# Optimization experiments

Hardware: AMD Instinct MI355X
Metric: run time of the kernel (lower is better)

The kernel has to match this reference:

```python
import jax, jax.numpy as jnp
import numpy as np

N_EMBD = 1024
N_HEAD = 16
HEAD_SIZE = N_EMBD // N_HEAD
EPS = 1e-5


def layernorm(x, g, b):
    mu = jnp.mean(x, axis=-1, keepdims=True)
    var = jnp.var(x, axis=-1, keepdims=True)
    return (x - mu) * jax.lax.rsqrt(var + EPS) * g + b


def setup_inputs() -> dict:
    key = jax.random.key(0)
    ks = jax.random.split(key, 12)
    s = 0.02
    C = N_EMBD
    return {
        "x": jax.random.normal(ks[0], (2, 2048, C), dtype=jnp.float32),
        "Wq": jax.random.normal(ks[1], (C, C), dtype=jnp.float32) * s,
        "Wk": jax.random.normal(ks[2], (C, C), dtype=jnp.float32) * s,
        "Wv": jax.random.normal(ks[3], (C, C), dtype=jnp.float32) * s,
        "Wo": jax.random.normal(ks[4], (C, C), dtype=jnp.float32) * s,
        "bo": jnp.zeros((C,), dtype=jnp.float32),
        "W1": jax.random.normal(ks[5], (C, 4 * C), dtype=jnp.float32) * s,
        "b1": jnp.zeros((4 * C,), dtype=jnp.float32),
        "W2": jax.random.normal(ks[6], (4 * C, C), dtype=jnp.float32) * s,
        "b2": jnp.zeros((C,), dtype=jnp.float32),
        "ln1_g": jnp.ones((C,), dtype=jnp.float32),
        "ln1_b": jnp.zeros((C,), dtype=jnp.float32),
        "ln2_g": jnp.ones((C,), dtype=jnp.float32),
        "ln2_b": jnp.zeros((C,), dtype=jnp.float32),
    }


def reference(x, Wq, Wk, Wv, Wo, bo, W1, b1, W2, b2, ln1_g, ln1_b, ln2_g, ln2_b):
    B, T, C = x.shape
    H, Dh = N_HEAD, HEAD_SIZE

    # --- self-attention branch ---
    h = layernorm(x, ln1_g, ln1_b)
    q = (h @ Wq).reshape(B, T, H, Dh)
    k = (h @ Wk).reshape(B, T, H, Dh)
    v = (h @ Wv).reshape(B, T, H, Dh)

    # NOTE: original scales by C**-0.5 (n_embd), not head_size**-0.5
    scale = C ** (-0.5)
    scores = jnp.einsum("bqhd,bkhd->bhqk", q, k) * scale  # [B,H,T,T]
    causal = jnp.tril(jnp.ones((T, T), dtype=bool))
    scores = jnp.where(causal, scores, -jnp.inf)
    wei = jax.nn.softmax(scores, axis=-1)
    attn = jnp.einsum("bhqk,bkhd->bqhd", wei, v).reshape(B, T, C)
    x = x + attn @ Wo + bo

    # --- MLP branch ---
    h2 = layernorm(x, ln2_g, ln2_b)
    ff = jax.nn.relu(h2 @ W1 + b1) @ W2 + b2
    return x + ff
```

## Files before the change

### kernel.cpp

```cpp
#include <hip/hip_runtime.h>

typedef unsigned short u16;
typedef __bf16 bf16;
typedef bf16 bf16x8 __attribute__((ext_vector_type(8)));
typedef float f32x4 __attribute__((ext_vector_type(4)));


__device__ __forceinline__ u16 f2bf(float f) {
  bf16 b = (bf16)f;
  return __builtin_bit_cast(u16, b);
}

__device__ __forceinline__ float fexp2(float x) {
#if __has_builtin(__builtin_amdgcn_exp2f)
  return __builtin_amdgcn_exp2f(x);
#else
  return exp2f(x);
#endif
}

__device__ __forceinline__ void gll16(void* lds, const void* g) {
  __builtin_amdgcn_global_load_lds((__attribute__((address_space(1))) void*)g,
                                   (__attribute__((address_space(3))) void*)lds,
                                   16, 0, 0);
}

__device__ __forceinline__ f32x4 mfma16(bf16x8 a, bf16x8 b, f32x4 c) {
  return __builtin_amdgcn_mfma_f32_16x16x32_bf16(a, b, c, 0, 0, 0);
}


__global__ __launch_bounds__(256)
void transpose_all(const float* __restrict__ Wq, const float* __restrict__ Wk,
                   const float* __restrict__ Wv, const float* __restrict__ Wo,
                   const float* __restrict__ W1, const float* __restrict__ W2,
                   u16* __restrict__ WqT, u16* __restrict__ WkT,
                   u16* __restrict__ WvT, u16* __restrict__ WoT,
                   u16* __restrict__ W1T, u16* __restrict__ W2T) {
  __shared__ float tile[32][33];
  const int id = blockIdx.x;
  const float* src;
  u16* dst;
  int R, C, t;
  if (id < 4096) {
    const int w = id >> 10;
    t = id & 1023; R = 1024; C = 1024;
    src = w == 0 ? Wq : w == 1 ? Wk : w == 2 ? Wv : Wo;
    dst = w == 0 ? WqT : w == 1 ? WkT : w == 2 ? WvT : WoT;
  } else if (id < 8192) {
    t = id - 4096; R = 1024; C = 4096; src = W1; dst = W1T;
  } else {
    t = id - 8192; R = 4096; C = 1024; src = W2; dst = W2T;
  }
  const int tilesx = C >> 5;
  const int c0 = (t % tilesx) * 32, r0 = (t / tilesx) * 32;
  const int tx = threadIdx.x, ty = threadIdx.y;
#pragma unroll
  for (int i = 0; i < 4; ++i)
    tile[ty + i * 8][tx] = src[(size_t)(r0 + ty + i * 8) * C + c0 + tx];
  __syncthreads();
#pragma unroll
  for (int i = 0; i < 4; ++i)
    dst[(size_t)(c0 + ty + i * 8) * R + r0 + tx] = f2bf(tile[tx][ty + i * 8]);
}


__global__ __launch_bounds__(256)
void ln_kernel(const float* __restrict__ x, const float* __restrict__ g,
               const float* __restrict__ bb, u16* __restrict__ h) {
  const int row = blockIdx.x;
  const int tid = threadIdx.x;
  const float4 xv = ((const float4*)(x + (size_t)row * 1024))[tid];
  float s = xv.x + xv.y + xv.z + xv.w;
  float q = xv.x * xv.x + xv.y * xv.y + xv.z * xv.z + xv.w * xv.w;
#pragma unroll
  for (int m = 1; m < 64; m <<= 1) {
    s += __shfl_xor(s, m);
    q += __shfl_xor(q, m);
  }
  __shared__ float ss[4], qq[4];
  const int wid = tid >> 6, lane = tid & 63;
  if (lane == 0) { ss[wid] = s; qq[wid] = q; }
  __syncthreads();
  s = ss[0] + ss[1] + ss[2] + ss[3];
  q = qq[0] + qq[1] + qq[2] + qq[3];
  const float mean = s * (1.0f / 1024.0f);
  const float var = q * (1.0f / 1024.0f) - mean * mean;
  const float rs = rsqrtf(var + 1e-5f);
  const float4 gv = ((const float4*)g)[tid];
  const float4 bv = ((const float4*)bb)[tid];
  ushort4 o;
  o.x = f2bf((xv.x - mean) * rs * gv.x + bv.x);
  o.y = f2bf((xv.y - mean) * rs * gv.y + bv.y);
  o.z = f2bf((xv.z - mean) * rs * gv.z + bv.z);
  o.w = f2bf((xv.w - mean) * rs * gv.w + bv.w);
  ((ushort4*)(h + (size_t)row * 1024))[tid] = o;
}


__device__ __forceinline__ void xcd_swizzle(int& bx, int& by, int& bz) {
  const int gx = gridDim.x, gy = gridDim.y;
  const int nwg = gx * gy * (int)gridDim.z;
  int flat = (int)blockIdx.x + gx * ((int)blockIdx.y + gy * (int)blockIdx.z);
  flat = (flat & 7) * (nwg >> 3) + (flat >> 3);
  bx = flat % gx;
  const int rem = flat / gx;
  by = rem % gy;
  bz = rem / gy;
}


template <int EPI>
__global__ __launch_bounds__(256)
void gemm_bt(const u16* __restrict__ A, const u16* __restrict__ Bt,
             const float* __restrict__ bias,
             void* __restrict__ O0, void* __restrict__ O1, void* __restrict__ O2,
             int M, int N, int K) {
  __shared__ __align__(16) u16 Alds[3][128 * 32];
  __shared__ __align__(16) u16 Blds[3][128 * 32];
  const int tid = threadIdx.x;
  const int lane = tid & 63, wid = tid >> 6;
  const int rl = lane & 15, kg = lane >> 4;
  const int ksw = (rl >> 1) & 3;
  int bx, by, bz;
  xcd_swizzle(bx, by, bz);
  const int m0 = by * 128, n0 = bx * 128;
  f32x4 acc[4][4];
#pragma unroll
  for (int i = 0; i < 4; ++i)
#pragma unroll
    for (int j = 0; j < 4; ++j) acc[i][j] = (f32x4){0.f, 0.f, 0.f, 0.f};
  const int wr = wid >> 1, wc = wid & 1;
  const int c0 = wid * 2, c1 = wid * 2 + 1;
  const int srow0 = c0 * 16 + (lane >> 2);
  const int srow1 = c1 * 16 + (lane >> 2);
  const int skol = (((lane & 3) ^ ((lane >> 3) & 3))) * 8;

#define STAGE_BT(buf, k0)                                                      \
  {                                                                            \
    gll16(Alds[buf] + c0 * 512, A + (size_t)(m0 + srow0) * K + (k0) + skol);   \
    gll16(Alds[buf] + c1 * 512, A + (size_t)(m0 + srow1) * K + (k0) + skol);   \
    gll16(Blds[buf] + c0 * 512, Bt + (size_t)(n0 + srow0) * K + (k0) + skol);  \
    gll16(Blds[buf] + c1 * 512, Bt + (size_t)(n0 + srow1) * K + (k0) + skol);  \
  }

  const int nt = K >> 5;
  STAGE_BT(0, 0);
  STAGE_BT(1, 32);
  int cur = 0;
  for (int t = 0; t < nt; ++t) {
    if (t + 1 < nt)
      asm volatile("s_waitcnt vmcnt(4)" ::: "memory");
    else
      asm volatile("s_waitcnt vmcnt(0)" ::: "memory");
    __builtin_amdgcn_s_barrier();
    if (t + 2 < nt) {
      const int nxt = cur >= 1 ? cur - 1 : cur + 2;
      STAGE_BT(nxt, (t + 2) << 5);
    }
    bf16x8 af[4], bfr[4];
#pragma unroll
    for (int m = 0; m < 4; ++m)
      af[m] = *(const bf16x8*)(Alds[cur] + (wr * 64 + m * 16 + rl) * 32 +
                               (kg ^ ksw) * 8);
#pragma unroll
    for (int n = 0; n < 4; ++n)
      bfr[n] = *(const bf16x8*)(Blds[cur] + (wc * 64 + n * 16 + rl) * 32 +
                                (kg ^ ksw) * 8);
    __builtin_amdgcn_s_setprio(1);
#pragma unroll
    for (int m = 0; m < 4; ++m)
#pragma unroll
      for (int n = 0; n < 4; ++n)
        acc[m][n] = mfma16(af[m], bfr[n], acc[m][n]);
    __builtin_amdgcn_s_setprio(0);
    cur = cur + 1 == 3 ? 0 : cur + 1;
  }
#undef STAGE_BT

#pragma unroll
  for (int m = 0; m < 4; ++m) {
#pragma unroll
    for (int n = 0; n < 4; ++n) {
      const int col = n0 + wc * 64 + n * 16 + rl;
      const int row0 = m0 + wr * 64 + m * 16 + kg * 4;
      if (EPI == 0) {
        const int seg = col >> 10;
        const int lc = col & 1023;
        if (seg == 2) {
          u16* vt = (u16*)O2;
          const size_t off =
              ((size_t)((row0 >> 11) * 16 + (lc >> 6)) * 64 + (lc & 63)) * 2048 +
              (row0 & 2047);
          ushort4 pk = {f2bf(acc[m][n][0]), f2bf(acc[m][n][1]),
                        f2bf(acc[m][n][2]), f2bf(acc[m][n][3])};
          *(ushort4*)(vt + off) = pk;
        } else {
          u16* o = (u16*)(seg == 0 ? O0 : O1);
#pragma unroll
          for (int r = 0; r < 4; ++r)
            o[(size_t)(row0 + r) * 1024 + lc] = f2bf(acc[m][n][r]);
        }
      } else {
        const float bv = bias[col];
#pragma unroll
        for (int r = 0; r < 4; ++r) {
          float v = acc[m][n][r] + bv;
          v = v > 0.f ? v : 0.f;
          ((u16*)O0)[(size_t)(row0 + r) * N + col] = f2bf(v);
        }
      }
    }
  }
}


__global__ __launch_bounds__(256)
void gemm64(const u16* __restrict__ A, const u16* __restrict__ Bt,
            const float* __restrict__ bias, const float* __restrict__ res,
            float* __restrict__ O, int M, int N, int K) {
  __shared__ __align__(16) u16 Alds[3][64 * 64];
  __shared__ __align__(16) u16 Blds[3][128 * 64];
  const int tid = threadIdx.x;
  const int lane = tid & 63, wid = tid >> 6;
  const int rl = lane & 15, kg = lane >> 4;
  int bx, by, bz;
  xcd_swizzle(bx, by, bz);
  const int m0 = by * 64, n0 = bx * 128;
  f32x4 acc[2][4];
#pragma unroll
  for (int i = 0; i < 2; ++i)
#pragma unroll
    for (int j = 0; j < 4; ++j) acc[i][j] = (f32x4){0.f, 0.f, 0.f, 0.f};
  const int wr = wid >> 1, wc = wid & 1;
  const int lrow = lane >> 3;
  const int lslot = lane & 7;

#define SRCA(base_r, k0)                                                       \
  (A + (size_t)(m0 + (base_r) + lrow) * K + (k0) +                             \
   ((lslot ^ (((base_r) + lrow) & 7)) * 8))
#define SRCB(base_r, k0)                                                       \
  (Bt + (size_t)(n0 + (base_r) + lrow) * K + (k0) +                            \
   ((lslot ^ (((base_r) + lrow) & 7)) * 8))

#define STAGE_64(buf, k0)                                                      \
  {                                                                            \
    gll16(Alds[buf] + (wid * 16 + 0) * 64, SRCA(wid * 16 + 0, k0));            \
    gll16(Alds[buf] + (wid * 16 + 8) * 64, SRCA(wid * 16 + 8, k0));            \
    gll16(Blds[buf] + (wid * 32 + 0) * 64, SRCB(wid * 32 + 0, k0));            \
    gll16(Blds[buf] + (wid * 32 + 8) * 64, SRCB(wid * 32 + 8, k0));            \
    gll16(Blds[buf] + (wid * 32 + 16) * 64, SRCB(wid * 32 + 16, k0));          \
    gll16(Blds[buf] + (wid * 32 + 24) * 64, SRCB(wid * 32 + 24, k0));          \
  }

  const int nt = K >> 6;
  STAGE_64(0, 0);
  STAGE_64(1, 64);
  int cur = 0;
  for (int t = 0; t < nt; ++t) {
    if (t + 1 < nt)
      asm volatile("s_waitcnt vmcnt(6)" ::: "memory");
    else
      asm volatile("s_waitcnt vmcnt(0)" ::: "memory");
    __builtin_amdgcn_s_barrier();
    if (t + 2 < nt) {
      const int nxt = cur >= 1 ? cur - 1 : cur + 2;
      STAGE_64(nxt, (t + 2) << 6);
    }
    bf16x8 af[2][2], bfr[4][2];
#pragma unroll
    for (int m = 0; m < 2; ++m) {
      const int row = wr * 32 + m * 16 + rl;
#pragma unroll
      for (int kf = 0; kf < 2; ++kf)
        af[m][kf] = *(const bf16x8*)(Alds[cur] + row * 64 +
                                     ((kf * 4 + kg) ^ (row & 7)) * 8);
    }
#pragma unroll
    for (int n = 0; n < 4; ++n) {
      const int row = wc * 64 + n * 16 + rl;
#pragma unroll
      for (int kf = 0; kf < 2; ++kf)
        bfr[n][kf] = *(const bf16x8*)(Blds[cur] + row * 64 +
                                      ((kf * 4 + kg) ^ (row & 7)) * 8);
    }
    __builtin_amdgcn_s_setprio(1);
#pragma unroll
    for (int m = 0; m < 2; ++m)
#pragma unroll
      for (int n = 0; n < 4; ++n) {
        acc[m][n] = mfma16(af[m][0], bfr[n][0], acc[m][n]);
        acc[m][n] = mfma16(af[m][1], bfr[n][1], acc[m][n]);
      }
    __builtin_amdgcn_s_setprio(0);
    cur = cur + 1 == 3 ? 0 : cur + 1;
  }
#undef STAGE_64
#undef SRCA
#undef SRCB

#pragma unroll
  for (int m = 0; m < 2; ++m) {
#pragma unroll
    for (int n = 0; n < 4; ++n) {
      const int col = n0 + wc * 64 + n * 16 + rl;
      const int row0 = m0 + wr * 32 + m * 16 + kg * 4;
      const float bv = bias[col];
#pragma unroll
      for (int r = 0; r < 4; ++r) {
        const int row = row0 + r;
        O[(size_t)row * N + col] =
            acc[m][n][r] + bv + res[(size_t)row * N + col];
      }
    }
  }
}


#define SC2 0.045084220027780106f

__device__ __forceinline__ void attn_range(
    const u16* __restrict__ qg, const u16* __restrict__ kgl,
    const u16* __restrict__ vtb, size_t rowb, int cb, char* plw,
    int rl, int kg, int q0, int kvb, int kve, bool mask_last,
    f32x4 (&ot)[2][4], float (&lrun)[2]) {
  if (kvb >= kve) return;
  const int swz = (rl & 7) << 4;
  bf16x8 qf[2][2];
#pragma unroll
  for (int m = 0; m < 2; ++m) {
    const u16* qp = qg + (rowb + q0 + m * 16 + rl) * 1024 + cb + kg * 8;
    qf[m][0] = *(const bf16x8*)(qp);
    qf[m][1] = *(const bf16x8*)(qp + 32);
  }

  bf16x8 ka[4][2], kb[4][2];
#define LOADK(dst, kvi)                                                        \
  {                                                                            \
    const u16* krow = kgl + (rowb + (kvi) * 64 + rl) * 1024 + cb + kg * 8;     \
    _Pragma("unroll") for (int n = 0; n < 4; ++n) {                            \
      dst[n][0] = *(const bf16x8*)(krow + (size_t)n * 16 * 1024);              \
      dst[n][1] = *(const bf16x8*)(krow + (size_t)n * 16 * 1024 + 32);         \
    }                                                                          \
  }

#define BODY(kf, kvi)                                                          \
  {                                                                            \
    const int kv0 = (kvi) * 64;                                                \
    const u16* vrow = vtb + (size_t)rl * 2048 + kv0 + kg * 8;                  \
    bf16x8 vfr[4][2];                                                          \
    _Pragma("unroll") for (int dt = 0; dt < 4; ++dt) {                         \
      vfr[dt][0] = *(const bf16x8*)(vrow + (size_t)dt * 16 * 2048);            \
      vfr[dt][1] = *(const bf16x8*)(vrow + (size_t)dt * 16 * 2048 + 32);       \
    }                                                                          \
    const bool domask = mask_last && ((kvi) == kve - 1);                       \
    _Pragma("unroll") for (int m = 0; m < 2; ++m) {                            \
      f32x4 s[4];                                                              \
      __builtin_amdgcn_s_setprio(1);                                           \
      _Pragma("unroll") for (int n = 0; n < 4; ++n) {                          \
        f32x4 t = (f32x4){0.f, 0.f, 0.f, 0.f};                                 \
        t = mfma16(kf[n][0], qf[m][0], t);                                     \
        t = mfma16(kf[n][1], qf[m][1], t);                                     \
        s[n] = t;                                                              \
      }                                                                        \
      __builtin_amdgcn_s_setprio(0);                                           \
      if (domask) {                                                            \
        const int qrow = q0 + m * 16 + rl;                                     \
        _Pragma("unroll") for (int n = 0; n < 4; ++n)                          \
            _Pragma("unroll") for (int r = 0; r < 4; ++r) {                    \
          const int tk = kv0 + n * 16 + 4 * kg + r;                            \
          s[n][r] = (tk > qrow) ? -3e38f : s[n][r];                            \
        }                                                                      \
      }                                                                        \
      float ps = 0.f;                                                          \
      _Pragma("unroll") for (int n = 0; n < 4; ++n) {                          \
        const float p0 = fexp2(__builtin_fmaf(s[n][0], SC2, -8.f));            \
        const float p1 = fexp2(__builtin_fmaf(s[n][1], SC2, -8.f));            \
        const float p2 = fexp2(__builtin_fmaf(s[n][2], SC2, -8.f));            \
        const float p3 = fexp2(__builtin_fmaf(s[n][3], SC2, -8.f));            \
        ps += (p0 + p1) + (p2 + p3);                                           \
        ushort4 pk = {f2bf(p0), f2bf(p1), f2bf(p2), f2bf(p3)};                 \
        *(ushort4*)(plw + m * 2048 + ((rl * 128 + n * 32 + kg * 8) ^ swz)) =   \
            pk;                                                                \
      }                                                                        \
      lrun[m] += ps;                                                           \
    }                                                                          \
    _Pragma("unroll") for (int m = 0; m < 2; ++m) {                            \
      const bf16x8 pf0 =                                                       \
          *(const bf16x8*)(plw + m * 2048 + ((rl * 128 + kg * 16) ^ swz));     \
      const bf16x8 pf1 = *(const bf16x8*)(plw + m * 2048 +                     \
                                          ((rl * 128 + 64 + kg * 16) ^ swz));  \
      __builtin_amdgcn_s_setprio(1);                                           \
      _Pragma("unroll") for (int dt = 0; dt < 4; ++dt) {                       \
        ot[m][dt] = mfma16(vfr[dt][0], pf0, ot[m][dt]);                        \
        ot[m][dt] = mfma16(vfr[dt][1], pf1, ot[m][dt]);                        \
      }                                                                        \
      __builtin_amdgcn_s_setprio(0);                                           \
    }                                                                          \
  }

  LOADK(ka, kvb);
  int kv = kvb;
  for (;;) {
    if (kv + 1 < kve) LOADK(kb, kv + 1);
    BODY(ka, kv);
    ++kv;
    if (kv >= kve) break;
    if (kv + 1 < kve) LOADK(ka, kv + 1);
    BODY(kb, kv);
    ++kv;
    if (kv >= kve) break;
  }
#undef LOADK
#undef BODY
}

__global__ __launch_bounds__(128)
void attn_kernel(const u16* __restrict__ qg, const u16* __restrict__ kgl,
                 const u16* __restrict__ vtg, u16* __restrict__ og) {
  const int tid = threadIdx.x, lane = tid & 63, wid = tid >> 6;
  const int rl = lane & 15, kg = lane >> 4;
  const int flat = blockIdx.x;
  const int bh = (flat & 7) * 4 + ((flat >> 3) & 3);
  const int pr = flat >> 5;
  const int jA = pr, jB = 63 - pr;
  const int nA = (jA >> 1) + 1, nB = (jB >> 1) + 1;
  const int a = (nB - nA) >> 1;
  const size_t rowb = (size_t)(bh >> 4) * 2048;
  const int cb = (bh & 15) * 64;
  const u16* vtb = vtg + (size_t)bh * 64 * 2048;

  __shared__ __align__(16) char Pl[2][4096];
  __shared__ __align__(16) float MrgO[2][4][64][4];
  __shared__ float MrgL[2][16];
  char* plw = Pl[wid];

  f32x4 ot[2][4];
  float lrun[2] = {0.f, 0.f};
#pragma unroll
  for (int m = 0; m < 2; ++m)
#pragma unroll
    for (int dt = 0; dt < 4; ++dt) ot[m][dt] = (f32x4){0.f, 0.f, 0.f, 0.f};

  if (wid == 0) {
    attn_range(qg, kgl, vtb, rowb, cb, plw, rl, kg, jA * 32, 0, nA, true,
               ot, lrun);
#pragma unroll
    for (int m = 0; m < 2; ++m) {
      lrun[m] += __shfl_xor(lrun[m], 16);
      lrun[m] += __shfl_xor(lrun[m], 32);
      const float inv = 1.f / lrun[m];
      u16* orow = og + (rowb + jA * 32 + m * 16 + rl) * 1024 + cb;
#pragma unroll
      for (int dt = 0; dt < 4; ++dt) {
        ushort4 ok = {f2bf(ot[m][dt][0] * inv), f2bf(ot[m][dt][1] * inv),
                      f2bf(ot[m][dt][2] * inv), f2bf(ot[m][dt][3] * inv)};
        *(ushort4*)(orow + dt * 16 + 4 * kg) = ok;
      }
      lrun[m] = 0.f;
#pragma unroll
      for (int dt = 0; dt < 4; ++dt) ot[m][dt] = (f32x4){0.f, 0.f, 0.f, 0.f};
    }
    attn_range(qg, kgl, vtb, rowb, cb, plw, rl, kg, jB * 32, 0, a, false,
               ot, lrun);
  } else {
    attn_range(qg, kgl, vtb, rowb, cb, plw, rl, kg, jB * 32, a, nB, true,
               ot, lrun);
#pragma unroll
    for (int m = 0; m < 2; ++m) {
      lrun[m] += __shfl_xor(lrun[m], 16);
      lrun[m] += __shfl_xor(lrun[m], 32);
#pragma unroll
      for (int dt = 0; dt < 4; ++dt)
        *(f32x4*)(&MrgO[m][dt][lane][0]) = ot[m][dt];
      if (kg == 0) MrgL[m][rl] = lrun[m];
    }
  }
  __syncthreads();
  if (wid == 0) {
#pragma unroll
    for (int m = 0; m < 2; ++m) {
      lrun[m] += __shfl_xor(lrun[m], 16);
      lrun[m] += __shfl_xor(lrun[m], 32);
      const float inv = 1.f / (lrun[m] + MrgL[m][rl]);
      u16* orow = og + (rowb + jB * 32 + m * 16 + rl) * 1024 + cb;
#pragma unroll
      for (int dt = 0; dt < 4; ++dt) {
        const f32x4 o1 = *(const f32x4*)(&MrgO[m][dt][lane][0]);
        ushort4 ok;
#pragma unroll
        for (int r = 0; r < 4; ++r)
          ((u16*)&ok)[r] = f2bf((ot[m][dt][r] + o1[r]) * inv);
        *(ushort4*)(orow + dt * 16 + 4 * kg) = ok;
      }
    }
  }
}


extern "C" void kernel_launch(void* const* d_in, const int* in_sizes, int n_in,
                              void* d_out, int out_size, void* d_ws, size_t ws_size,
                              hipStream_t stream) {
  const float* x    = (const float*)d_in[0];
  const float* Wq   = (const float*)d_in[1];
  const float* Wk   = (const float*)d_in[2];
  const float* Wv   = (const float*)d_in[3];
  const float* Wo   = (const float*)d_in[4];
  const float* bo   = (const float*)d_in[5];
  const float* W1   = (const float*)d_in[6];
  const float* b1   = (const float*)d_in[7];
  const float* W2   = (const float*)d_in[8];
  const float* b2   = (const float*)d_in[9];
  const float* ln1g = (const float*)d_in[10];
  const float* ln1b = (const float*)d_in[11];
  const float* ln2g = (const float*)d_in[12];
  const float* ln2b = (const float*)d_in[13];
  float* out = (float*)d_out;

  char* ws = (char*)d_ws;
  const size_t MB = 1024 * 1024;
  u16* WqT  = (u16*)(ws + 0 * MB);
  u16* WoT  = (u16*)(ws + 6 * MB);
  u16* W1T  = (u16*)(ws + 8 * MB);
  u16* W2T  = (u16*)(ws + 16 * MB);
  u16* h    = (u16*)(ws + 24 * MB);
  u16* q    = (u16*)(ws + 32 * MB);
  u16* k    = (u16*)(ws + 40 * MB);
  u16* vt   = (u16*)(ws + 48 * MB);
  u16* attn = (u16*)(ws + 56 * MB);
  float* x1 = (float*)(ws + 64 * MB);
  u16* ff1  = (u16*)(ws + 32 * MB);
  u16* WkT  = WqT + 1024 * 1024;
  u16* WvT  = WqT + 2 * 1024 * 1024;

  dim3 tblk(32, 8);
  transpose_all<<<12288, tblk, 0, stream>>>(Wq, Wk, Wv, Wo, W1, W2,
                                            WqT, WkT, WvT, WoT, W1T, W2T);

  ln_kernel<<<4096, 256, 0, stream>>>(x, ln1g, ln1b, h);

  gemm_bt<0><<<dim3(24, 32), 256, 0, stream>>>(h, WqT, nullptr,
                                               q, k, vt, 4096, 3072, 1024);

  attn_kernel<<<1024, 128, 0, stream>>>(q, k, vt, attn);

  gemm64<<<dim3(8, 64), 256, 0, stream>>>(attn, WoT, bo, x, x1,
                                          4096, 1024, 1024);

  ln_kernel<<<4096, 256, 0, stream>>>(x1, ln2g, ln2b, h);

  gemm_bt<1><<<dim3(32, 32), 256, 0, stream>>>(h, W1T, b1, ff1, ff1, ff1,
                                               4096, 4096, 1024);

  gemm64<<<dim3(8, 64), 256, 0, stream>>>(ff1, W2T, b2, x1, out,
                                          4096, 1024, 4096);
}
```

Baseline: 253.3 us.

## Software-pipeline attention QK^T ahead of softmax and store residual x1 in bf16

The attention inner loop is restructured so the QK^T MFMAs for the next KV tile run while the current tile's softmax and PV are processed. K loads are issued two tiles ahead, with V loaded per step, to overlap memory latency with compute at the cost of extra score registers. Separately, the post-attention residual x1 is stored as bf16 instead of fp32, which halves its write and two reads but adds rounding error to the residual stream.

```diff
diff --git a/kernel.cpp b/kernel.cpp
--- a/kernel.cpp
+++ b/kernel.cpp
@@ -9,6 +9,10 @@
 __device__ __forceinline__ u16 f2bf(float f) {
   bf16 b = (bf16)f;
   return __builtin_bit_cast(u16, b);
+}
+
+__device__ __forceinline__ float b2f(u16 u) {
+  return __uint_as_float(((unsigned)u) << 16);
 }
 
 __device__ __forceinline__ float fexp2(float x) {
@@ -65,12 +69,19 @@
 }
 
 
+template <int BF16IN>
 __global__ __launch_bounds__(256)
-void ln_kernel(const float* __restrict__ x, const float* __restrict__ g,
+void ln_kernel(const void* __restrict__ xin, const float* __restrict__ g,
                const float* __restrict__ bb, u16* __restrict__ h) {
   const int row = blockIdx.x;
   const int tid = threadIdx.x;
-  const float4 xv = ((const float4*)(x + (size_t)row * 1024))[tid];
+  float4 xv;
+  if (BF16IN) {
+    const ushort4 u = ((const ushort4*)((const u16*)xin + (size_t)row * 1024))[tid];
+    xv.x = b2f(u.x); xv.y = b2f(u.y); xv.z = b2f(u.z); xv.w = b2f(u.w);
+  } else {
+    xv = ((const float4*)((const float*)xin + (size_t)row * 1024))[tid];
+  }
   float s = xv.x + xv.y + xv.z + xv.w;
   float q = xv.x * xv.x + xv.y * xv.y + xv.z * xv.z + xv.w * xv.w;
 #pragma unroll
@@ -215,10 +226,11 @@
 }
 
 
+template <int EPI>
 __global__ __launch_bounds__(256)
 void gemm64(const u16* __restrict__ A, const u16* __restrict__ Bt,
-            const float* __restrict__ bias, const float* __restrict__ res,
-            float* __restrict__ O, int M, int N, int K) {
+            const float* __restrict__ bias, const void* __restrict__ res,
+            void* __restrict__ O, int M, int N, int K) {
   __shared__ __align__(16) u16 Alds[3][64 * 64];
   __shared__ __align__(16) u16 Blds[3][128 * 64];
   const int tid = threadIdx.x;
@@ -309,8 +321,13 @@
 #pragma unroll
       for (int r = 0; r < 4; ++r) {
         const int row = row0 + r;
-        O[(size_t)row * N + col] =
-            acc[m][n][r] + bv + res[(size_t)row * N + col];
+        if (EPI == 0) {
+          const float rv = ((const float*)res)[(size_t)row * N + col];
+          ((u16*)O)[(size_t)row * N + col] = f2bf(acc[m][n][r] + bv + rv);
+        } else {
+          const float rv = b2f(((const u16*)res)[(size_t)row * N + col]);
+          ((float*)O)[(size_t)row * N + col] = acc[m][n][r] + bv + rv;
+        }
       }
     }
   }
@@ -334,7 +351,9 @@
     qf[m][1] = *(const bf16x8*)(qp + 32);
   }
 
-  bf16x8 ka[4][2], kb[4][2];
+  bf16x8 ka[4][2], kb[4][2], vf[4][2];
+  f32x4 sa[2][4], sb[2][4];
+
 #define LOADK(dst, kvi)                                                        \
   {                                                                            \
     const u16* krow = kgl + (rowb + (kvi) * 64 + rl) * 1024 + cb + kg * 8;     \
@@ -344,40 +363,47 @@
     }                                                                          \
   }
 
-#define BODY(kf, kvi)                                                          \
+#define LOADV(kvi)                                                             \
+  {                                                                            \
+    const u16* vrow = vtb + (size_t)rl * 2048 + (kvi) * 64 + kg * 8;           \
+    _Pragma("unroll") for (int dt = 0; dt < 4; ++dt) {                         \
+      vf[dt][0] = *(const bf16x8*)(vrow + (size_t)dt * 16 * 2048);             \
+      vf[dt][1] = *(const bf16x8*)(vrow + (size_t)dt * 16 * 2048 + 32);        \
+    }                                                                          \
+  }
+
+#define QKC(S, KF)                                                             \
+  {                                                                            \
+    __builtin_amdgcn_s_setprio(1);                                             \
+    _Pragma("unroll") for (int m = 0; m < 2; ++m)                              \
+        _Pragma("unroll") for (int n = 0; n < 4; ++n) {                        \
+      f32x4 t = (f32x4){0.f, 0.f, 0.f, 0.f};                                   \
+      t = mfma16(KF[n][0], qf[m][0], t);                                       \
+      t = mfma16(KF[n][1], qf[m][1], t);                                       \
+      S[m][n] = t;                                                             \
+    }                                                                          \
+    __builtin_amdgcn_s_setprio(0);                                             \
+  }
+
+#define SMAX(S, kvi)                                                           \
   {                                                                            \
     const int kv0 = (kvi) * 64;                                                \
-    const u16* vrow = vtb + (size_t)rl * 2048 + kv0 + kg * 8;                  \
-    bf16x8 vfr[4][2];                                                          \
-    _Pragma("unroll") for (int dt = 0; dt < 4; ++dt) {                         \
-      vfr[dt][0] = *(const bf16x8*)(vrow + (size_t)dt * 16 * 2048);            \
-      vfr[dt][1] = *(const bf16x8*)(vrow + (size_t)dt * 16 * 2048 + 32);       \
-    }                                                                          \
     const bool domask = mask_last && ((kvi) == kve - 1);                       \
     _Pragma("unroll") for (int m = 0; m < 2; ++m) {                            \
-      f32x4 s[4];                                                              \
-      __builtin_amdgcn_s_setprio(1);                                           \
-      _Pragma("unroll") for (int n = 0; n < 4; ++n) {                          \
-        f32x4 t = (f32x4){0.f, 0.f, 0.f, 0.f};                                 \
-        t = mfma16(kf[n][0], qf[m][0], t);                                     \
-        t = mfma16(kf[n][1], qf[m][1], t);                                     \
-        s[n] = t;                                                              \
-      }                                                                        \
-      __builtin_amdgcn_s_setprio(0);                                           \
       if (domask) {                                                            \
         const int qrow = q0 + m * 16 + rl;                                     \
         _Pragma("unroll") for (int n = 0; n < 4; ++n)                          \
             _Pragma("unroll") for (int r = 0; r < 4; ++r) {                    \
           const int tk = kv0 + n * 16 + 4 * kg + r;                            \
-          s[n][r] = (tk > qrow) ? -3e38f : s[n][r];                            \
+          S[m][n][r] = (tk > qrow) ? -3e38f : S[m][n][r];                      \
         }                                                                      \
       }                                                                        \
       float ps = 0.f;                                                          \
       _Pragma("unroll") for (int n = 0; n < 4; ++n) {                          \
-        const float p0 = fexp2(__builtin_fmaf(s[n][0], SC2, -8.f));            \
-        const float p1 = fexp2(__builtin_fmaf(s[n][1], SC2, -8.f));            \
-        const float p2 = fexp2(__builtin_fmaf(s[n][2], SC2, -8.f));            \
-        const float p3 = fexp2(__builtin_fmaf(s[n][3], SC2, -8.f));            \
+        const float p0 = fexp2(__builtin_fmaf(S[m][n][0], SC2, -8.f));         \
+        const float p1 = fexp2(__builtin_fmaf(S[m][n][1], SC2, -8.f));         \
+        const float p2 = fexp2(__builtin_fmaf(S[m][n][2], SC2, -8.f));         \
+        const float p3 = fexp2(__builtin_fmaf(S[m][n][3], SC2, -8.f));         \
         ps += (p0 + p1) + (p2 + p3);                                           \
         ushort4 pk = {f2bf(p0), f2bf(p1), f2bf(p2), f2bf(p3)};                 \
         *(ushort4*)(plw + m * 2048 + ((rl * 128 + n * 32 + kg * 8) ^ swz)) =   \
@@ -385,6 +411,10 @@
       }                                                                        \
       lrun[m] += ps;                                                           \
     }                                                                          \
+  }
+
+#define PVC()                                                                  \
+  {                                                                            \
     _Pragma("unroll") for (int m = 0; m < 2; ++m) {                            \
       const bf16x8 pf0 =                                                       \
           *(const bf16x8*)(plw + m * 2048 + ((rl * 128 + kg * 16) ^ swz));     \
@@ -392,27 +422,40 @@
                                           ((rl * 128 + 64 + kg * 16) ^ swz));  \
       __builtin_amdgcn_s_setprio(1);                                           \
       _Pragma("unroll") for (int dt = 0; dt < 4; ++dt) {                       \
-        ot[m][dt] = mfma16(vfr[dt][0], pf0, ot[m][dt]);                        \
-        ot[m][dt] = mfma16(vfr[dt][1], pf1, ot[m][dt]);                        \
+        ot[m][dt] = mfma16(vf[dt][0], pf0, ot[m][dt]);                         \
+        ot[m][dt] = mfma16(vf[dt][1], pf1, ot[m][dt]);                         \
       }                                                                        \
       __builtin_amdgcn_s_setprio(0);                                           \
     }                                                                          \
   }
 
+#define STEP(SC_, SN_, KN_, KC_, kvi)                                          \
+  {                                                                            \
+    LOADV(kvi);                                                                \
+    SMAX(SC_, kvi);                                                            \
+    if ((kvi) + 1 < kve) QKC(SN_, KN_);                                        \
+    if ((kvi) + 2 < kve) LOADK(KC_, (kvi) + 2);                                \
+    PVC();                                                                     \
+  }
+
   LOADK(ka, kvb);
+  if (kvb + 1 < kve) LOADK(kb, kvb + 1);
+  QKC(sa, ka);
   int kv = kvb;
   for (;;) {
-    if (kv + 1 < kve) LOADK(kb, kv + 1);
-    BODY(ka, kv);
+    STEP(sa, sb, kb, ka, kv);
     ++kv;
     if (kv >= kve) break;
-    if (kv + 1 < kve) LOADK(ka, kv + 1);
-    BODY(kb, kv);
+    STEP(sb, sa, ka, kb, kv);
     ++kv;
     if (kv >= kve) break;
   }
 #undef LOADK
-#undef BODY
+#undef LOADV
+#undef QKC
+#undef SMAX
+#undef PVC
+#undef STEP
 }
 
 __global__ __launch_bounds__(128)
@@ -528,7 +571,7 @@
   u16* k    = (u16*)(ws + 40 * MB);
   u16* vt   = (u16*)(ws + 48 * MB);
   u16* attn = (u16*)(ws + 56 * MB);
-  float* x1 = (float*)(ws + 64 * MB);
+  u16* x1b  = (u16*)(ws + 64 * MB);
   u16* ff1  = (u16*)(ws + 32 * MB);
   u16* WkT  = WqT + 1024 * 1024;
   u16* WvT  = WqT + 2 * 1024 * 1024;
@@ -537,21 +580,21 @@
   transpose_all<<<12288, tblk, 0, stream>>>(Wq, Wk, Wv, Wo, W1, W2,
                                             WqT, WkT, WvT, WoT, W1T, W2T);
 
-  ln_kernel<<<4096, 256, 0, stream>>>(x, ln1g, ln1b, h);
+  ln_kernel<0><<<4096, 256, 0, stream>>>(x, ln1g, ln1b, h);
 
   gemm_bt<0><<<dim3(24, 32), 256, 0, stream>>>(h, WqT, nullptr,
                                                q, k, vt, 4096, 3072, 1024);
 
   attn_kernel<<<1024, 128, 0, stream>>>(q, k, vt, attn);
 
-  gemm64<<<dim3(8, 64), 256, 0, stream>>>(attn, WoT, bo, x, x1,
-                                          4096, 1024, 1024);
-
-  ln_kernel<<<4096, 256, 0, stream>>>(x1, ln2g, ln2b, h);
+  gemm64<0><<<dim3(8, 64), 256, 0, stream>>>(attn, WoT, bo, x, x1b,
+                                             4096, 1024, 1024);
+
+  ln_kernel<1><<<4096, 256, 0, stream>>>(x1b, ln2g, ln2b, h);
 
   gemm_bt<1><<<dim3(32, 32), 256, 0, stream>>>(h, W1T, b1, ff1, ff1, ff1,
                                                4096, 4096, 1024);
 
-  gemm64<<<dim3(8, 64), 256, 0, stream>>>(ff1, W2T, b2, x1, out,
-                                          4096, 1024, 4096);
-}
+  gemm64<1><<<dim3(8, 64), 256, 0, stream>>>(ff1, W2T, b2, x1b, out,
+                                             4096, 1024, 4096);
+}
```

After: 252.9 us. About the same (-0.2%).

## Use 256x128 GEMM tiles with 8 waves and store residual x1 in bf16

Applied to the files above, without the earlier changes.

The QKV and FF1 GEMMs move from 128x128 tiles with 4 waves to 256x128 tiles with 8 waves (512 threads). Each wave still computes a 64x64 sub-tile, and the staging loads and vmcnt counts are adjusted to match. The goal is more reuse of the B operand per block and less global traffic. The intermediate residual x1 is now written as bf16 rather than fp32, which halves its write and its two reads (by LN2 and the final residual add). The trade-offs are fewer blocks per grid, which may hurt load balance across CUs, and reduced precision in the residual path.

```diff
diff --git a/kernel.cpp b/kernel.cpp
--- a/kernel.cpp
+++ b/kernel.cpp
@@ -9,6 +9,10 @@
 __device__ __forceinline__ u16 f2bf(float f) {
   bf16 b = (bf16)f;
   return __builtin_bit_cast(u16, b);
+}
+
+__device__ __forceinline__ float b2f(u16 u) {
+  return __uint_as_float(((unsigned)u) << 16);
 }
 
 __device__ __forceinline__ float fexp2(float x) {
@@ -65,12 +69,19 @@
 }
 
 
+template <int BF16IN>
 __global__ __launch_bounds__(256)
-void ln_kernel(const float* __restrict__ x, const float* __restrict__ g,
+void ln_kernel(const void* __restrict__ xin, const float* __restrict__ g,
                const float* __restrict__ bb, u16* __restrict__ h) {
   const int row = blockIdx.x;
   const int tid = threadIdx.x;
-  const float4 xv = ((const float4*)(x + (size_t)row * 1024))[tid];
+  float4 xv;
+  if (BF16IN) {
+    const ushort4 u = ((const ushort4*)((const u16*)xin + (size_t)row * 1024))[tid];
+    xv.x = b2f(u.x); xv.y = b2f(u.y); xv.z = b2f(u.z); xv.w = b2f(u.w);
+  } else {
+    xv = ((const float4*)((const float*)xin + (size_t)row * 1024))[tid];
+  }
   float s = xv.x + xv.y + xv.z + xv.w;
   float q = xv.x * xv.x + xv.y * xv.y + xv.z * xv.z + xv.w * xv.w;
 #pragma unroll
@@ -111,12 +122,12 @@
 
 
 template <int EPI>
-__global__ __launch_bounds__(256)
-void gemm_bt(const u16* __restrict__ A, const u16* __restrict__ Bt,
+__global__ __launch_bounds__(512)
+void gemm256(const u16* __restrict__ A, const u16* __restrict__ Bt,
              const float* __restrict__ bias,
              void* __restrict__ O0, void* __restrict__ O1, void* __restrict__ O2,
              int M, int N, int K) {
-  __shared__ __align__(16) u16 Alds[3][128 * 32];
+  __shared__ __align__(16) u16 Alds[3][256 * 32];
   __shared__ __align__(16) u16 Blds[3][128 * 32];
   const int tid = threadIdx.x;
   const int lane = tid & 63, wid = tid >> 6;
@@ -124,39 +135,39 @@
   const int ksw = (rl >> 1) & 3;
   int bx, by, bz;
   xcd_swizzle(bx, by, bz);
-  const int m0 = by * 128, n0 = bx * 128;
+  const int m0 = by * 256, n0 = bx * 128;
   f32x4 acc[4][4];
 #pragma unroll
   for (int i = 0; i < 4; ++i)
 #pragma unroll
     for (int j = 0; j < 4; ++j) acc[i][j] = (f32x4){0.f, 0.f, 0.f, 0.f};
   const int wr = wid >> 1, wc = wid & 1;
-  const int c0 = wid * 2, c1 = wid * 2 + 1;
-  const int srow0 = c0 * 16 + (lane >> 2);
-  const int srow1 = c1 * 16 + (lane >> 2);
+  const int srow = lane >> 2;
   const int skol = (((lane & 3) ^ ((lane >> 3) & 3))) * 8;
 
-#define STAGE_BT(buf, k0)                                                      \
+#define STAGE_256(buf, k0)                                                     \
   {                                                                            \
-    gll16(Alds[buf] + c0 * 512, A + (size_t)(m0 + srow0) * K + (k0) + skol);   \
-    gll16(Alds[buf] + c1 * 512, A + (size_t)(m0 + srow1) * K + (k0) + skol);   \
-    gll16(Blds[buf] + c0 * 512, Bt + (size_t)(n0 + srow0) * K + (k0) + skol);  \
-    gll16(Blds[buf] + c1 * 512, Bt + (size_t)(n0 + srow1) * K + (k0) + skol);  \
+    gll16(Alds[buf] + (wid * 32 + 0) * 32,                                     \
+          A + (size_t)(m0 + wid * 32 + 0 + srow) * K + (k0) + skol);           \
+    gll16(Alds[buf] + (wid * 32 + 16) * 32,                                    \
+          A + (size_t)(m0 + wid * 32 + 16 + srow) * K + (k0) + skol);          \
+    gll16(Blds[buf] + (wid * 16) * 32,                                         \
+          Bt + (size_t)(n0 + wid * 16 + srow) * K + (k0) + skol);              \
   }
 
   const int nt = K >> 5;
-  STAGE_BT(0, 0);
-  STAGE_BT(1, 32);
+  STAGE_256(0, 0);
+  STAGE_256(1, 32);
   int cur = 0;
   for (int t = 0; t < nt; ++t) {
     if (t + 1 < nt)
-      asm volatile("s_waitcnt vmcnt(4)" ::: "memory");
+      asm volatile("s_waitcnt vmcnt(3)" ::: "memory");
     else
       asm volatile("s_waitcnt vmcnt(0)" ::: "memory");
     __builtin_amdgcn_s_barrier();
     if (t + 2 < nt) {
       const int nxt = cur >= 1 ? cur - 1 : cur + 2;
-      STAGE_BT(nxt, (t + 2) << 5);
+      STAGE_256(nxt, (t + 2) << 5);
     }
     bf16x8 af[4], bfr[4];
 #pragma unroll
@@ -176,7 +187,7 @@
     __builtin_amdgcn_s_setprio(0);
     cur = cur + 1 == 3 ? 0 : cur + 1;
   }
-#undef STAGE_BT
+#undef STAGE_256
 
 #pragma unroll
   for (int m = 0; m < 4; ++m) {
@@ -215,10 +226,11 @@
 }
 
 
+template <int EPI>
 __global__ __launch_bounds__(256)
 void gemm64(const u16* __restrict__ A, const u16* __restrict__ Bt,
-            const float* __restrict__ bias, const float* __restrict__ res,
-            float* __restrict__ O, int M, int N, int K) {
+            const float* __restrict__ bias, const void* __restrict__ res,
+            void* __restrict__ O, int M, int N, int K) {
   __shared__ __align__(16) u16 Alds[3][64 * 64];
   __shared__ __align__(16) u16 Blds[3][128 * 64];
   const int tid = threadIdx.x;
@@ -309,8 +321,13 @@
 #pragma unroll
       for (int r = 0; r < 4; ++r) {
         const int row = row0 + r;
-        O[(size_t)row * N + col] =
-            acc[m][n][r] + bv + res[(size_t)row * N + col];
+        if (EPI == 0) {
+          const float rv = ((const float*)res)[(size_t)row * N + col];
+          ((u16*)O)[(size_t)row * N + col] = f2bf(acc[m][n][r] + bv + rv);
+        } else {
+          const float rv = b2f(((const u16*)res)[(size_t)row * N + col]);
+          ((float*)O)[(size_t)row * N + col] = acc[m][n][r] + bv + rv;
+        }
       }
     }
   }
@@ -528,7 +545,7 @@
   u16* k    = (u16*)(ws + 40 * MB);
   u16* vt   = (u16*)(ws + 48 * MB);
   u16* attn = (u16*)(ws + 56 * MB);
-  float* x1 = (float*)(ws + 64 * MB);
+  u16* x1b  = (u16*)(ws + 64 * MB);
   u16* ff1  = (u16*)(ws + 32 * MB);
   u16* WkT  = WqT + 1024 * 1024;
   u16* WvT  = WqT + 2 * 1024 * 1024;
@@ -537,21 +554,21 @@
   transpose_all<<<12288, tblk, 0, stream>>>(Wq, Wk, Wv, Wo, W1, W2,
                                             WqT, WkT, WvT, WoT, W1T, W2T);
 
-  ln_kernel<<<4096, 256, 0, stream>>>(x, ln1g, ln1b, h);
-
-  gemm_bt<0><<<dim3(24, 32), 256, 0, stream>>>(h, WqT, nullptr,
+  ln_kernel<0><<<4096, 256, 0, stream>>>(x, ln1g, ln1b, h);
+
+  gemm256<0><<<dim3(24, 16), 512, 0, stream>>>(h, WqT, nullptr,
                                                q, k, vt, 4096, 3072, 1024);
 
   attn_kernel<<<1024, 128, 0, stream>>>(q, k, vt, attn);
 
-  gemm64<<<dim3(8, 64), 256, 0, stream>>>(attn, WoT, bo, x, x1,
-                                          4096, 1024, 1024);
-
-  ln_kernel<<<4096, 256, 0, stream>>>(x1, ln2g, ln2b, h);
-
-  gemm_bt<1><<<dim3(32, 32), 256, 0, stream>>>(h, W1T, b1, ff1, ff1, ff1,
+  gemm64<0><<<dim3(8, 64), 256, 0, stream>>>(attn, WoT, bo, x, x1b,
+                                             4096, 1024, 1024);
+
+  ln_kernel<1><<<4096, 256, 0, stream>>>(x1b, ln2g, ln2b, h);
+
+  gemm256<1><<<dim3(32, 16), 512, 0, stream>>>(h, W1T, b1, ff1, ff1, ff1,
                                                4096, 4096, 1024);
 
-  gemm64<<<dim3(8, 64), 256, 0, stream>>>(ff1, W2T, b2, x1, out,
-                                          4096, 1024, 4096);
-}
+  gemm64<1><<<dim3(8, 64), 256, 0, stream>>>(ff1, W2T, b2, x1b, out,
+                                             4096, 1024, 4096);
+}
```

After: 239.2 us. -5.6%, faster.
